# Optimization experiments

Measured on AMD Instinct MI355X. Metric: run time of the kernel, lower is better.

The kernel has to match this reference:

```python
import jax, jax.numpy as jnp
import numpy as np

B, L, D = 2, 2048, 1024
H, DK, DV = 16, 64, 64
EPS = 1e-6


def setup_inputs() -> dict:
    key = jax.random.key(0)
    ks = jax.random.split(key, 7)
    s = 0.02
    return {
        "x": jax.random.normal(ks[0], (B, L, D), dtype=jnp.float32),
        "Wq": jax.random.normal(ks[1], (D, H * DK), dtype=jnp.float32) * s,
        "Wk": jax.random.normal(ks[2], (D, H * DK), dtype=jnp.float32) * s,
        "Wv": jax.random.normal(ks[3], (D, H * DV), dtype=jnp.float32) * s,
        "Wo": jax.random.normal(ks[4], (H * DV, D), dtype=jnp.float32) * s,
        "ln_gamma": jnp.ones((D,), dtype=jnp.float32),
        "ln_beta": jnp.zeros((D,), dtype=jnp.float32),
    }


def reference(x, Wq, Wk, Wv, Wo, ln_gamma, ln_beta):
    temp = jnp.asarray(DK, x.dtype) ** 0.5
    # projections -> [B, H, L, Dh]
    q = (x @ Wq).reshape(B, L, H, DK).transpose(0, 2, 1, 3)
    k = (x @ Wk).reshape(B, L, H, DK).transpose(0, 2, 1, 3)
    v = (x @ Wv).reshape(B, L, H, DV).transpose(0, 2, 1, 3)
    # naive attention: explicit [B,H,L,L] scores (dropout rate 0 -> identity)
    scores = jnp.einsum("bhqd,bhkd->bhqk", q / temp, k)
    attn = jax.nn.softmax(scores, axis=-1)
    o = jnp.einsum("bhqk,bhkd->bhqd", attn, v)
    o = o.transpose(0, 2, 1, 3).reshape(B, L, H * DV)
    out = o @ Wo + x  # residual
    # LayerNorm(eps=1e-6)
    mu = jnp.mean(out, axis=-1, keepdims=True)
    var = jnp.var(out, axis=-1, keepdims=True)
    return (out - mu) * jax.lax.rsqrt(var + EPS) * ln_gamma + ln_beta
```

## Files before the change

### kernel.cpp

```cpp
#include <hip/hip_runtime.h>


typedef __bf16 bf16;
typedef __bf16 bf16x2 __attribute__((ext_vector_type(2)));
typedef __bf16 bf16x4 __attribute__((ext_vector_type(4)));
typedef __bf16 bf16x8 __attribute__((ext_vector_type(8)));
typedef float floatx4 __attribute__((ext_vector_type(4)));
typedef int intx4 __attribute__((ext_vector_type(4)));

#define MFMA16(a, b, c) __builtin_amdgcn_mfma_f32_16x16x32_bf16((a), (b), (c), 0, 0, 0)

__global__ __launch_bounds__(256) void k_prep_x(const float* __restrict__ x, bf16* __restrict__ xb) {
  const int i = (blockIdx.x * 256 + threadIdx.x) * 4;
  const float4 v = *reinterpret_cast<const float4*>(x + i);
  bf16x4 o = {(bf16)v.x, (bf16)v.y, (bf16)v.z, (bf16)v.w};
  *reinterpret_cast<bf16x4*>(xb + i) = o;
}

__global__ __launch_bounds__(256) void k_prep_w(const float* __restrict__ Wq, const float* __restrict__ Wk,
                                                const float* __restrict__ Wv, const float* __restrict__ Wo,
                                                bf16* __restrict__ WT) {
  __shared__ float tile[32][33];
  const int z = blockIdx.z;
  const float* W = (z == 0) ? Wq : (z == 1) ? Wk : (z == 2) ? Wv : Wo;
  const int n0 = blockIdx.x * 32, k0 = blockIdx.y * 32;
  const int tx = threadIdx.x, ty = threadIdx.y;
#pragma unroll
  for (int j = 0; j < 32; j += 8)
    tile[ty + j][tx] = W[(size_t)(k0 + ty + j) * 1024 + n0 + tx];
  __syncthreads();
#pragma unroll
  for (int j = 0; j < 32; j += 8)
    WT[(size_t)(z * 1024 + n0 + ty + j) * 1024 + k0 + tx] = (bf16)tile[tx][ty + j];
}

template <int MODE>
__global__ __launch_bounds__(256) void k_gemm(const bf16* __restrict__ A, const bf16* __restrict__ Bt,
                                              const float* __restrict__ X, float* __restrict__ Y,
                                              bf16* __restrict__ QB, bf16* __restrict__ KB,
                                              bf16* __restrict__ VTB) {
  __shared__ __align__(16) bf16 As[128 * 72];
  __shared__ __align__(16) bf16 Bs[128 * 72];
  const int t = threadIdx.x;
  const int lane = t & 63, wv = t >> 6;
  const int qd = lane >> 4, col = lane & 15;
  const int wm = wv >> 1, wn = wv & 1;
  const int m0 = blockIdx.x * 128, n0 = blockIdx.y * 128;
  const int srow = t >> 3, sc = (t & 7) * 8;

  floatx4 acc[4][4] = {};

  bf16x8 av[4], bv[4];
#pragma unroll
  for (int j = 0; j < 4; j++) {
    av[j] = *reinterpret_cast<const bf16x8*>(A + (size_t)(m0 + srow + j * 32) * 1024 + sc);
    bv[j] = *reinterpret_cast<const bf16x8*>(Bt + (size_t)(n0 + srow + j * 32) * 1024 + sc);
  }

  for (int kt = 0; kt < 1024; kt += 64) {
    __syncthreads();
#pragma unroll
    for (int j = 0; j < 4; j++) {
      *reinterpret_cast<bf16x8*>(As + (srow + j * 32) * 72 + sc) = av[j];
      *reinterpret_cast<bf16x8*>(Bs + (srow + j * 32) * 72 + sc) = bv[j];
    }
    __syncthreads();
    const int ktn = (kt + 64) & 1023;
#pragma unroll
    for (int j = 0; j < 4; j++) {
      av[j] = *reinterpret_cast<const bf16x8*>(A + (size_t)(m0 + srow + j * 32) * 1024 + ktn + sc);
      bv[j] = *reinterpret_cast<const bf16x8*>(Bt + (size_t)(n0 + srow + j * 32) * 1024 + ktn + sc);
    }
#pragma unroll
    for (int ks = 0; ks < 2; ks++) {
      bf16x8 af[4], bfr[4];
#pragma unroll
      for (int i = 0; i < 4; i++)
        af[i] = *reinterpret_cast<const bf16x8*>(As + (wm * 64 + i * 16 + col) * 72 + ks * 32 + qd * 8);
#pragma unroll
      for (int i = 0; i < 4; i++)
        bfr[i] = *reinterpret_cast<const bf16x8*>(Bs + (wn * 64 + i * 16 + col) * 72 + ks * 32 + qd * 8);
#pragma unroll
      for (int i = 0; i < 4; i++)
#pragma unroll
        for (int j = 0; j < 4; j++)
          acc[i][j] = MFMA16(af[i], bfr[j], acc[i][j]);
    }
  }

#pragma unroll
  for (int i = 0; i < 4; i++) {
#pragma unroll
    for (int j = 0; j < 4; j++) {
      const int mb = m0 + wm * 64 + i * 16 + qd * 4;
      const int n = n0 + wn * 64 + j * 16 + col;
      if (MODE == 0) {
        const int seg = n >> 10;
        const int h = (n & 1023) >> 6, dd = n & 63;
#pragma unroll
        for (int r = 0; r < 4; r++) {
          const int m = mb + r;
          const int bb = m >> 11, l = m & 2047;
          const float v = acc[i][j][r];
          if (seg == 0)
            QB[((size_t)(bb * 16 + h) * 2048 + l) * 64 + dd] = (bf16)(v * 0.125f);
          else if (seg == 1)
            KB[((size_t)(bb * 16 + h) * 2048 + l) * 64 + dd] = (bf16)v;
          else
            VTB[((size_t)(bb * 16 + h) * 64 + dd) * 2048 + l] = (bf16)v;
        }
      } else {
#pragma unroll
        for (int r = 0; r < 4; r++) {
          const int m = mb + r;
          Y[(size_t)m * 1024 + n] = acc[i][j][r] + X[(size_t)m * 1024 + n];
        }
      }
    }
  }
}

__global__ __launch_bounds__(256) void k_attn(const bf16* __restrict__ QB, const bf16* __restrict__ KB,
                                              const bf16* __restrict__ VTB, bf16* __restrict__ OB) {
  __shared__ __align__(16) bf16 Ks[64 * 72];
  __shared__ __align__(16) bf16 Vs[64 * 72];
  const int t = threadIdx.x;
  const int lane = t & 63, wv = t >> 6;
  const int qd = lane >> 4, col = lane & 15;
  const int bh = blockIdx.y;
  const int qr = blockIdx.x * 128 + wv * 32;
  const int srow = t >> 3, sc = (t & 7) * 8;
  const int krow0 = (((srow >> 2) & 1) << 4) + (((srow >> 3) & 3) << 2) + (srow & 3);

  bf16x8 bQ[2][2];
#pragma unroll
  for (int qt = 0; qt < 2; qt++)
#pragma unroll
    for (int s = 0; s < 2; s++)
      bQ[qt][s] = *reinterpret_cast<const bf16x8*>(QB + ((size_t)bh * 2048 + qr + qt * 16 + col) * 64 + s * 32 + qd * 8);

  floatx4 oacc[2][4] = {};
  float lsum[2] = {0.f, 0.f};

  bf16x8 kv0 = *reinterpret_cast<const bf16x8*>(KB + ((size_t)bh * 2048 + srow) * 64 + sc);
  bf16x8 kv1 = *reinterpret_cast<const bf16x8*>(KB + ((size_t)bh * 2048 + srow + 32) * 64 + sc);
  bf16x8 vv0 = *reinterpret_cast<const bf16x8*>(VTB + ((size_t)bh * 64 + srow) * 2048 + sc);
  bf16x8 vv1 = *reinterpret_cast<const bf16x8*>(VTB + ((size_t)bh * 64 + srow + 32) * 2048 + sc);

  for (int kt = 0; kt < 2048; kt += 64) {
    __syncthreads();
    *reinterpret_cast<bf16x8*>(Ks + krow0 * 72 + sc) = kv0;
    *reinterpret_cast<bf16x8*>(Ks + (krow0 + 32) * 72 + sc) = kv1;
    *reinterpret_cast<bf16x8*>(Vs + srow * 72 + sc) = vv0;
    *reinterpret_cast<bf16x8*>(Vs + (srow + 32) * 72 + sc) = vv1;
    __syncthreads();
    const int ktn = (kt + 64) & 2047;
    kv0 = *reinterpret_cast<const bf16x8*>(KB + ((size_t)bh * 2048 + ktn + srow) * 64 + sc);
    kv1 = *reinterpret_cast<const bf16x8*>(KB + ((size_t)bh * 2048 + ktn + srow + 32) * 64 + sc);
    vv0 = *reinterpret_cast<const bf16x8*>(VTB + ((size_t)bh * 64 + srow) * 2048 + ktn + sc);
    vv1 = *reinterpret_cast<const bf16x8*>(VTB + ((size_t)bh * 64 + srow + 32) * 2048 + ktn + sc);

    bf16x8 aK[4][2];
#pragma unroll
    for (int nt = 0; nt < 4; nt++)
#pragma unroll
      for (int s = 0; s < 2; s++)
        aK[nt][s] = *reinterpret_cast<const bf16x8*>(Ks + (nt * 16 + col) * 72 + s * 32 + qd * 8);

    int pk[2][4][2];
#pragma unroll
    for (int qt = 0; qt < 2; qt++) {
#pragma unroll
      for (int nt = 0; nt < 4; nt++) {
        floatx4 z = {0.f, 0.f, 0.f, 0.f};
#pragma unroll
        for (int s = 0; s < 2; s++) z = MFMA16(aK[nt][s], bQ[qt][s], z);
        const float e0 = __expf(z[0]), e1 = __expf(z[1]), e2 = __expf(z[2]), e3 = __expf(z[3]);
        lsum[qt] += (e0 + e1) + (e2 + e3);
        bf16x2 p01, p23;
        p01[0] = (bf16)e0; p01[1] = (bf16)e1;
        p23[0] = (bf16)e2; p23[1] = (bf16)e3;
        pk[qt][nt][0] = __builtin_bit_cast(int, p01);
        pk[qt][nt][1] = __builtin_bit_cast(int, p23);
      }
    }

    bf16x8 bV[4][2];
#pragma unroll
    for (int nd = 0; nd < 4; nd++)
#pragma unroll
      for (int s = 0; s < 2; s++)
        bV[nd][s] = *reinterpret_cast<const bf16x8*>(Vs + (nd * 16 + col) * 72 + s * 32 + qd * 8);

#pragma unroll
    for (int qt = 0; qt < 2; qt++)
#pragma unroll
      for (int s = 0; s < 2; s++) {
        intx4 w;
        w[0] = pk[qt][2 * s][0]; w[1] = pk[qt][2 * s][1];
        w[2] = pk[qt][2 * s + 1][0]; w[3] = pk[qt][2 * s + 1][1];
        const bf16x8 aP = __builtin_bit_cast(bf16x8, w);
#pragma unroll
        for (int nd = 0; nd < 4; nd++)
          oacc[qt][nd] = MFMA16(aP, bV[nd][s], oacc[qt][nd]);
      }
  }

#pragma unroll
  for (int qt = 0; qt < 2; qt++) {
    lsum[qt] += __shfl_xor(lsum[qt], 16);
    lsum[qt] += __shfl_xor(lsum[qt], 32);
  }
  const int bb = bh >> 4, h = bh & 15;
#pragma unroll
  for (int qt = 0; qt < 2; qt++) {
#pragma unroll
    for (int r = 0; r < 4; r++) {
      const float linv = 1.f / __shfl(lsum[qt], qd * 4 + r);
      const size_t m = (size_t)bb * 2048 + qr + qt * 16 + qd * 4 + r;
#pragma unroll
      for (int nd = 0; nd < 4; nd++)
        OB[m * 1024 + h * 64 + nd * 16 + col] = (bf16)(oacc[qt][nd][r] * linv);
    }
  }
}

__global__ __launch_bounds__(256) void k_ln(const float* __restrict__ Yin, const float* __restrict__ gamma,
                                            const float* __restrict__ beta, float* __restrict__ out) {
  __shared__ float red[8];
  const int row = blockIdx.x, t = threadIdx.x;
  const float4 v = *reinterpret_cast<const float4*>(Yin + (size_t)row * 1024 + t * 4);
  float s = v.x + v.y + v.z + v.w;
  float ss = v.x * v.x + v.y * v.y + v.z * v.z + v.w * v.w;
#pragma unroll
  for (int d = 1; d < 64; d <<= 1) {
    s += __shfl_xor(s, d);
    ss += __shfl_xor(ss, d);
  }
  if ((t & 63) == 0) {
    red[t >> 6] = s;
    red[4 + (t >> 6)] = ss;
  }
  __syncthreads();
  s = red[0] + red[1] + red[2] + red[3];
  ss = red[4] + red[5] + red[6] + red[7];
  const float mu = s * (1.f / 1024.f);
  const float var = ss * (1.f / 1024.f) - mu * mu;
  const float rs = rsqrtf(var + 1e-6f);
  const float4 g = *reinterpret_cast<const float4*>(gamma + t * 4);
  const float4 bt = *reinterpret_cast<const float4*>(beta + t * 4);
  float4 o;
  o.x = (v.x - mu) * rs * g.x + bt.x;
  o.y = (v.y - mu) * rs * g.y + bt.y;
  o.z = (v.z - mu) * rs * g.z + bt.z;
  o.w = (v.w - mu) * rs * g.w + bt.w;
  *reinterpret_cast<float4*>(out + (size_t)row * 1024 + t * 4) = o;
}

extern "C" void kernel_launch(void* const* d_in, const int* in_sizes, int n_in,
                              void* d_out, int out_size, void* d_ws, size_t ws_size,
                              hipStream_t stream) {
  (void)in_sizes; (void)n_in; (void)out_size; (void)ws_size;
  const float* x = (const float*)d_in[0];
  const float* Wq = (const float*)d_in[1];
  const float* Wk = (const float*)d_in[2];
  const float* Wv = (const float*)d_in[3];
  const float* Wo = (const float*)d_in[4];
  const float* gamma = (const float*)d_in[5];
  const float* beta = (const float*)d_in[6];

  char* ws = (char*)d_ws;
  const size_t MB = 1ull << 20;
  bf16* XB = (bf16*)(ws);
  bf16* OB = (bf16*)(ws);
  bf16* WT = (bf16*)(ws + 8 * MB);
  bf16* QB = (bf16*)(ws + 16 * MB);
  bf16* KB = (bf16*)(ws + 24 * MB);
  bf16* VTB = (bf16*)(ws + 32 * MB);
  float* Y = (float*)(ws + 16 * MB);

  k_prep_x<<<4096, 256, 0, stream>>>(x, XB);
  k_prep_w<<<dim3(32, 32, 4), dim3(32, 8), 0, stream>>>(Wq, Wk, Wv, Wo, WT);
  k_gemm<0><<<dim3(32, 24), 256, 0, stream>>>(XB, WT, nullptr, nullptr, QB, KB, VTB);
  k_attn<<<dim3(16, 32), 256, 0, stream>>>(QB, KB, VTB, OB);
  k_gemm<1><<<dim3(32, 8), 256, 0, stream>>>(OB, WT + (size_t)3072 * 1024, x, Y,
                                             nullptr, nullptr, nullptr);
  k_ln<<<4096, 256, 0, stream>>>(Y, gamma, beta, (float*)d_out);
}
```

Measured before the change: 210.5 us.

## Use direct global-to-LDS loads and software-pipeline attention QK/PV across buffers

Replaces register-staged global loads with direct global_load_lds copies in both the GEMM and attention kernels, and drops the padded LDS row stride. The attention loop gains double-buffered K/V tiles and a software pipeline in which the QK MFMAs for the next tile overlap the exp/pack and PV of the previous tile. Removing the padding risks LDS bank conflicts on the fragment reads. The GEMM loses its register prefetch, so its global loads are now exposed between barriers.

```diff
diff --git a/kernel.cpp b/kernel.cpp
--- a/kernel.cpp
+++ b/kernel.cpp
@@ -9,6 +9,11 @@
 typedef int intx4 __attribute__((ext_vector_type(4)));
 
 #define MFMA16(a, b, c) __builtin_amdgcn_mfma_f32_16x16x32_bf16((a), (b), (c), 0, 0, 0)
+
+__device__ __forceinline__ void gll16(const bf16* g, bf16* l) {
+  __builtin_amdgcn_global_load_lds((const __attribute__((address_space(1))) void*)g,
+                                   (__attribute__((address_space(3))) void*)l, 16, 0, 0);
+}
 
 __global__ __launch_bounds__(256) void k_prep_x(const float* __restrict__ x, bf16* __restrict__ xb) {
   const int i = (blockIdx.x * 256 + threadIdx.x) * 4;
@@ -39,47 +44,37 @@
                                               const float* __restrict__ X, float* __restrict__ Y,
                                               bf16* __restrict__ QB, bf16* __restrict__ KB,
                                               bf16* __restrict__ VTB) {
-  __shared__ __align__(16) bf16 As[128 * 72];
-  __shared__ __align__(16) bf16 Bs[128 * 72];
+  __shared__ __align__(16) bf16 As[128 * 64];
+  __shared__ __align__(16) bf16 Bs[128 * 64];
   const int t = threadIdx.x;
   const int lane = t & 63, wv = t >> 6;
   const int qd = lane >> 4, col = lane & 15;
   const int wm = wv >> 1, wn = wv & 1;
   const int m0 = blockIdx.x * 128, n0 = blockIdx.y * 128;
-  const int srow = t >> 3, sc = (t & 7) * 8;
+  const int srow = wv * 8 + (lane >> 3);
+  const int scol = (lane & 7) * 8;
+  const bf16* Ag = A + (size_t)(m0 + srow) * 1024 + scol;
+  const bf16* Bg = Bt + (size_t)(n0 + srow) * 1024 + scol;
 
   floatx4 acc[4][4] = {};
-
-  bf16x8 av[4], bv[4];
-#pragma unroll
-  for (int j = 0; j < 4; j++) {
-    av[j] = *reinterpret_cast<const bf16x8*>(A + (size_t)(m0 + srow + j * 32) * 1024 + sc);
-    bv[j] = *reinterpret_cast<const bf16x8*>(Bt + (size_t)(n0 + srow + j * 32) * 1024 + sc);
-  }
 
   for (int kt = 0; kt < 1024; kt += 64) {
     __syncthreads();
 #pragma unroll
-    for (int j = 0; j < 4; j++) {
-      *reinterpret_cast<bf16x8*>(As + (srow + j * 32) * 72 + sc) = av[j];
-      *reinterpret_cast<bf16x8*>(Bs + (srow + j * 32) * 72 + sc) = bv[j];
+    for (int rd = 0; rd < 4; rd++) {
+      gll16(Ag + (size_t)rd * 32 * 1024 + kt, As + (rd * 32 + wv * 8) * 64);
+      gll16(Bg + (size_t)rd * 32 * 1024 + kt, Bs + (rd * 32 + wv * 8) * 64);
     }
     __syncthreads();
-    const int ktn = (kt + 64) & 1023;
-#pragma unroll
-    for (int j = 0; j < 4; j++) {
-      av[j] = *reinterpret_cast<const bf16x8*>(A + (size_t)(m0 + srow + j * 32) * 1024 + ktn + sc);
-      bv[j] = *reinterpret_cast<const bf16x8*>(Bt + (size_t)(n0 + srow + j * 32) * 1024 + ktn + sc);
-    }
 #pragma unroll
     for (int ks = 0; ks < 2; ks++) {
       bf16x8 af[4], bfr[4];
 #pragma unroll
       for (int i = 0; i < 4; i++)
-        af[i] = *reinterpret_cast<const bf16x8*>(As + (wm * 64 + i * 16 + col) * 72 + ks * 32 + qd * 8);
+        af[i] = *reinterpret_cast<const bf16x8*>(As + (wm * 64 + i * 16 + col) * 64 + ks * 32 + qd * 8);
 #pragma unroll
       for (int i = 0; i < 4; i++)
-        bfr[i] = *reinterpret_cast<const bf16x8*>(Bs + (wn * 64 + i * 16 + col) * 72 + ks * 32 + qd * 8);
+        bfr[i] = *reinterpret_cast<const bf16x8*>(Bs + (wn * 64 + i * 16 + col) * 64 + ks * 32 + qd * 8);
 #pragma unroll
       for (int i = 0; i < 4; i++)
 #pragma unroll
@@ -122,15 +117,22 @@
 
 __global__ __launch_bounds__(256) void k_attn(const bf16* __restrict__ QB, const bf16* __restrict__ KB,
                                               const bf16* __restrict__ VTB, bf16* __restrict__ OB) {
-  __shared__ __align__(16) bf16 Ks[64 * 72];
-  __shared__ __align__(16) bf16 Vs[64 * 72];
+  __shared__ __align__(16) bf16 Ks[2][64 * 64];
+  __shared__ __align__(16) bf16 Vs[2][64 * 64];
   const int t = threadIdx.x;
   const int lane = t & 63, wv = t >> 6;
   const int qd = lane >> 4, col = lane & 15;
   const int bh = blockIdx.y;
   const int qr = blockIdx.x * 128 + wv * 32;
-  const int srow = t >> 3, sc = (t & 7) * 8;
-  const int krow0 = (((srow >> 2) & 1) << 4) + (((srow >> 3) & 3) << 2) + (srow & 3);
+  const int lrow0 = wv * 8 + (lane >> 3);
+  const int scol = (lane & 7) * 8;
+  const int kg0 = ((lrow0 >> 5) << 5) + (((lrow0 >> 2) & 3) << 3) + (((lrow0 >> 4) & 1) << 2) + (lrow0 & 3);
+  const int r1 = lrow0 + 32;
+  const int kg1 = ((r1 >> 5) << 5) + (((r1 >> 2) & 3) << 3) + (((r1 >> 4) & 1) << 2) + (r1 & 3);
+  const bf16* Kg0 = KB + ((size_t)bh * 2048 + kg0) * 64 + scol;
+  const bf16* Kg1 = KB + ((size_t)bh * 2048 + kg1) * 64 + scol;
+  const bf16* Vg0 = VTB + ((size_t)bh * 64 + lrow0) * 2048 + scol;
+  const bf16* Vg1 = VTB + ((size_t)bh * 64 + lrow0 + 32) * 2048 + scol;
 
   bf16x8 bQ[2][2];
 #pragma unroll
@@ -141,70 +143,82 @@
 
   floatx4 oacc[2][4] = {};
   float lsum[2] = {0.f, 0.f};
-
-  bf16x8 kv0 = *reinterpret_cast<const bf16x8*>(KB + ((size_t)bh * 2048 + srow) * 64 + sc);
-  bf16x8 kv1 = *reinterpret_cast<const bf16x8*>(KB + ((size_t)bh * 2048 + srow + 32) * 64 + sc);
-  bf16x8 vv0 = *reinterpret_cast<const bf16x8*>(VTB + ((size_t)bh * 64 + srow) * 2048 + sc);
-  bf16x8 vv1 = *reinterpret_cast<const bf16x8*>(VTB + ((size_t)bh * 64 + srow + 32) * 2048 + sc);
-
-  for (int kt = 0; kt < 2048; kt += 64) {
+  floatx4 scur[2][4];
+  int pk[2][4][2];
+
+#define STAGE(i)                                                      \
+  do {                                                                \
+    const int b_ = (i) & 1;                                           \
+    gll16(Kg0 + (size_t)(i) * 4096, &Ks[b_][(wv * 8) * 64]);          \
+    gll16(Kg1 + (size_t)(i) * 4096, &Ks[b_][(32 + wv * 8) * 64]);     \
+    gll16(Vg0 + (i) * 64, &Vs[b_][(wv * 8) * 64]);                    \
+    gll16(Vg1 + (i) * 64, &Vs[b_][(32 + wv * 8) * 64]);               \
+  } while (0)
+
+#define QK(i)                                                                                   \
+  do {                                                                                          \
+    const bf16* ks_ = Ks[(i) & 1];                                                              \
+    _Pragma("unroll") for (int nt = 0; nt < 4; nt++) {                                          \
+      bf16x8 a0 = *reinterpret_cast<const bf16x8*>(ks_ + (nt * 16 + col) * 64 + qd * 8);        \
+      bf16x8 a1 = *reinterpret_cast<const bf16x8*>(ks_ + (nt * 16 + col) * 64 + 32 + qd * 8);   \
+      _Pragma("unroll") for (int qt = 0; qt < 2; qt++) {                                        \
+        floatx4 z = {0.f, 0.f, 0.f, 0.f};                                                       \
+        z = MFMA16(a0, bQ[qt][0], z);                                                           \
+        z = MFMA16(a1, bQ[qt][1], z);                                                           \
+        scur[qt][nt] = z;                                                                       \
+      }                                                                                         \
+    }                                                                                           \
+  } while (0)
+
+#define EXPPACK()                                                                               \
+  do {                                                                                          \
+    _Pragma("unroll") for (int qt = 0; qt < 2; qt++) {                                          \
+      _Pragma("unroll") for (int nt = 0; nt < 4; nt++) {                                        \
+        const float e0 = __expf(scur[qt][nt][0]), e1 = __expf(scur[qt][nt][1]);                 \
+        const float e2 = __expf(scur[qt][nt][2]), e3 = __expf(scur[qt][nt][3]);                 \
+        lsum[qt] += (e0 + e1) + (e2 + e3);                                                      \
+        bf16x2 p01, p23;                                                                        \
+        p01[0] = (bf16)e0; p01[1] = (bf16)e1;                                                   \
+        p23[0] = (bf16)e2; p23[1] = (bf16)e3;                                                   \
+        pk[qt][nt][0] = __builtin_bit_cast(int, p01);                                           \
+        pk[qt][nt][1] = __builtin_bit_cast(int, p23);                                           \
+      }                                                                                         \
+    }                                                                                           \
+  } while (0)
+
+#define PV(i)                                                                                   \
+  do {                                                                                          \
+    const bf16* vs_ = Vs[(i) & 1];                                                              \
+    bf16x8 bV[4][2];                                                                            \
+    _Pragma("unroll") for (int nd = 0; nd < 4; nd++) {                                          \
+      bV[nd][0] = *reinterpret_cast<const bf16x8*>(vs_ + (nd * 16 + col) * 64 + qd * 8);        \
+      bV[nd][1] = *reinterpret_cast<const bf16x8*>(vs_ + (nd * 16 + col) * 64 + 32 + qd * 8);   \
+    }                                                                                           \
+    _Pragma("unroll") for (int qt = 0; qt < 2; qt++) {                                          \
+      _Pragma("unroll") for (int s = 0; s < 2; s++) {                                           \
+        intx4 w;                                                                                \
+        w[0] = pk[qt][2 * s][0]; w[1] = pk[qt][2 * s][1];                                       \
+        w[2] = pk[qt][2 * s + 1][0]; w[3] = pk[qt][2 * s + 1][1];                               \
+        const bf16x8 aP = __builtin_bit_cast(bf16x8, w);                                        \
+        _Pragma("unroll") for (int nd = 0; nd < 4; nd++)                                        \
+          oacc[qt][nd] = MFMA16(aP, bV[nd][s], oacc[qt][nd]);                                   \
+      }                                                                                         \
+    }                                                                                           \
+  } while (0)
+
+  STAGE(0);
+  __syncthreads();
+  QK(0);
+  for (int i = 1; i < 32; i++) {
     __syncthreads();
-    *reinterpret_cast<bf16x8*>(Ks + krow0 * 72 + sc) = kv0;
-    *reinterpret_cast<bf16x8*>(Ks + (krow0 + 32) * 72 + sc) = kv1;
-    *reinterpret_cast<bf16x8*>(Vs + srow * 72 + sc) = vv0;
-    *reinterpret_cast<bf16x8*>(Vs + (srow + 32) * 72 + sc) = vv1;
+    STAGE(i);
+    EXPPACK();
+    PV(i - 1);
     __syncthreads();
-    const int ktn = (kt + 64) & 2047;
-    kv0 = *reinterpret_cast<const bf16x8*>(KB + ((size_t)bh * 2048 + ktn + srow) * 64 + sc);
-    kv1 = *reinterpret_cast<const bf16x8*>(KB + ((size_t)bh * 2048 + ktn + srow + 32) * 64 + sc);
-    vv0 = *reinterpret_cast<const bf16x8*>(VTB + ((size_t)bh * 64 + srow) * 2048 + ktn + sc);
-    vv1 = *reinterpret_cast<const bf16x8*>(VTB + ((size_t)bh * 64 + srow + 32) * 2048 + ktn + sc);
-
-    bf16x8 aK[4][2];
-#pragma unroll
-    for (int nt = 0; nt < 4; nt++)
-#pragma unroll
-      for (int s = 0; s < 2; s++)
-        aK[nt][s] = *reinterpret_cast<const bf16x8*>(Ks + (nt * 16 + col) * 72 + s * 32 + qd * 8);
-
-    int pk[2][4][2];
-#pragma unroll
-    for (int qt = 0; qt < 2; qt++) {
-#pragma unroll
-      for (int nt = 0; nt < 4; nt++) {
-        floatx4 z = {0.f, 0.f, 0.f, 0.f};
-#pragma unroll
-        for (int s = 0; s < 2; s++) z = MFMA16(aK[nt][s], bQ[qt][s], z);
-        const float e0 = __expf(z[0]), e1 = __expf(z[1]), e2 = __expf(z[2]), e3 = __expf(z[3]);
-        lsum[qt] += (e0 + e1) + (e2 + e3);
-        bf16x2 p01, p23;
-        p01[0] = (bf16)e0; p01[1] = (bf16)e1;
-        p23[0] = (bf16)e2; p23[1] = (bf16)e3;
-        pk[qt][nt][0] = __builtin_bit_cast(int, p01);
-        pk[qt][nt][1] = __builtin_bit_cast(int, p23);
-      }
-    }
-
-    bf16x8 bV[4][2];
-#pragma unroll
-    for (int nd = 0; nd < 4; nd++)
-#pragma unroll
-      for (int s = 0; s < 2; s++)
-        bV[nd][s] = *reinterpret_cast<const bf16x8*>(Vs + (nd * 16 + col) * 72 + s * 32 + qd * 8);
-
-#pragma unroll
-    for (int qt = 0; qt < 2; qt++)
-#pragma unroll
-      for (int s = 0; s < 2; s++) {
-        intx4 w;
-        w[0] = pk[qt][2 * s][0]; w[1] = pk[qt][2 * s][1];
-        w[2] = pk[qt][2 * s + 1][0]; w[3] = pk[qt][2 * s + 1][1];
-        const bf16x8 aP = __builtin_bit_cast(bf16x8, w);
-#pragma unroll
-        for (int nd = 0; nd < 4; nd++)
-          oacc[qt][nd] = MFMA16(aP, bV[nd][s], oacc[qt][nd]);
-      }
-  }
+    QK(i);
+  }
+  EXPPACK();
+  PV(31);
 
 #pragma unroll
   for (int qt = 0; qt < 2; qt++) {
@@ -223,6 +237,10 @@
         OB[m * 1024 + h * 64 + nd * 16 + col] = (bf16)(oacc[qt][nd][r] * linv);
     }
   }
+#undef STAGE
+#undef QK
+#undef EXPPACK
+#undef PV
 }
 
 __global__ __launch_bounds__(256) void k_ln(const float* __restrict__ Yin, const float* __restrict__ gamma,
```

Measured after the change: 230.9 us. 1.1x slower.
